# Optimization experiments

Measured on AMD Instinct MI355X. Metric: run time of the kernel, lower is better.

## Reference

```python
import jax, jax.numpy as jnp
import numpy as np

B, N, D = 8192, 50, 64


def setup_inputs() -> dict:
    key = jax.random.key(0)
    k1, k2, k3 = jax.random.split(key, 3)
    F = jax.random.normal(k1, (B, N, D), dtype=jnp.float32)
    # xavier_normal for square DxD linear: std = sqrt(2/(D+D)) = 1/sqrt(D)
    std = 1.0 / np.sqrt(D)
    K_w = jax.random.normal(k2, (D, D), dtype=jnp.float32) * std
    Q_w = jax.random.normal(k3, (D, D), dtype=jnp.float32) * std
    return {"F": F, "K_w": K_w, "Q_w": Q_w}


def reference(F, K_w, Q_w):
    # K(F): Linear with weight K_w (torch convention: x @ W^T)
    KF = jnp.einsum('bnd,ed->bne', F, K_w)          # [B,N,D]
    # S = F @ K(F)^T
    S = jnp.einsum('bnd,bmd->bnm', F, KF)           # [B,N,N]
    # out[b,n,d] = sum_m S[b,n,m] * F[b,n,d] * F[b,m,d]
    #            = F[b,n,d] * (S @ F)[b,n,d]   (algebraic fusion of the
    #              bnd,bmd->bnmd outer product + weighted sum over m)
    out = F * jnp.einsum('bnm,bmd->bnd', S, F)      # [B,N,D]
    # residual branch: Q(F)
    out = out + jnp.einsum('bnd,ed->bne', F, Q_w)
    return out
```

## Files before the change

kernel.cpp:

```cpp
#include <hip/hip_runtime.h>

typedef __attribute__((ext_vector_type(8))) short s16x8;
typedef __attribute__((ext_vector_type(4))) short s16x4;
typedef __attribute__((ext_vector_type(4))) float f32x4;

#define ST 72
#define NB 8
#define MFMA __builtin_amdgcn_mfma_f32_16x16x32_bf16

__device__ __forceinline__ short f2bf(float f) {
    unsigned u = __builtin_bit_cast(unsigned, f);
    u += 0x7FFFu + ((u >> 16) & 1u);
    return (short)(u >> 16);
}
__device__ __forceinline__ s16x8 cvt8(f32x4 a, f32x4 b) {
    s16x8 r = { f2bf(a.x), f2bf(a.y), f2bf(a.z), f2bf(a.w),
                f2bf(b.x), f2bf(b.y), f2bf(b.z), f2bf(b.w) };
    return r;
}

__global__ __launch_bounds__(256, 4) void sam3e_v2(
    const float* __restrict__ F, const float* __restrict__ Kw,
    const float* __restrict__ Qw, float* __restrict__ out)
{
    __shared__ __align__(16) short sKw[64 * ST];
    __shared__ __align__(16) short sQw[64 * ST];
    __shared__ __align__(16) short sAT[64 * ST];
    __shared__ __align__(16) short sKS[64 * ST];

    const int tid  = threadIdx.x;
    const int w    = tid >> 6;
    const int lane = tid & 63;
    const int col  = lane & 15;
    const int q    = lane >> 4;

    {
        const int e  = tid & 63;
        const int dg = tid >> 6;
        const f32x4* Kv = (const f32x4*)(Kw + e * 64 + dg * 16);
        const f32x4* Qv = (const f32x4*)(Qw + e * 64 + dg * 16);
        #pragma unroll
        for (int k = 0; k < 4; ++k) {
            f32x4 kv = Kv[k], qv = Qv[k];
            s16x4 hk = { f2bf(kv.x), f2bf(kv.y), f2bf(kv.z), f2bf(kv.w) };
            s16x4 hq = { f2bf(qv.x), f2bf(qv.y), f2bf(qv.z), f2bf(qv.w) };
            *(s16x4*)&sKw[e * ST + dg * 16 + k * 4] = hk;
            *(s16x4*)&sQw[e * ST + dg * 16 + k * 4] = hq;
        }
    }

    const int sn  = tid & 63;
    const int sdg = tid >> 6;
    const f32x4 z4 = {0.f, 0.f, 0.f, 0.f};

    int b = blockIdx.x * NB;
    f32x4 pf0 = z4, pf1 = z4, pf2 = z4, pf3 = z4;
    if (sn < 50) {
        const f32x4* Fr = (const f32x4*)(F + (size_t)b * 3200 + sn * 64 + sdg * 16);
        pf0 = Fr[0]; pf1 = Fr[1]; pf2 = Fr[2]; pf3 = Fr[3];
    }

    for (int it = 0; it < NB; ++it, ++b) {
        const float* Fb = F   + (size_t)b * 3200;
        float*       Ob = out + (size_t)b * 3200;

        __syncthreads();

        {
            const int d0 = sdg * 16;
            short h[16] = { f2bf(pf0.x), f2bf(pf0.y), f2bf(pf0.z), f2bf(pf0.w),
                            f2bf(pf1.x), f2bf(pf1.y), f2bf(pf1.z), f2bf(pf1.w),
                            f2bf(pf2.x), f2bf(pf2.y), f2bf(pf2.z), f2bf(pf2.w),
                            f2bf(pf3.x), f2bf(pf3.y), f2bf(pf3.z), f2bf(pf3.w) };
            #pragma unroll
            for (int i = 0; i < 16; ++i) sAT[(d0 + i) * ST + sn] = h[i];
        }

        s16x8 a0, a1;
        {
            const int row = 16 * w + col;
            f32x4 v0 = z4, v1 = z4, v2 = z4, v3 = z4;
            if (row < 50) {
                const f32x4* Fr = (const f32x4*)(Fb + row * 64);
                v0 = Fr[2 * q]; v1 = Fr[2 * q + 1];
                v2 = Fr[8 + 2 * q]; v3 = Fr[8 + 2 * q + 1];
            }
            a0 = cvt8(v0, v1); a1 = cvt8(v2, v3);
        }

        #pragma unroll
        for (int nt = 0; nt < 4; ++nt) {
            const short* yb = &sKw[(16 * nt + col) * ST + 8 * q];
            f32x4 acc = {0.f, 0.f, 0.f, 0.f};
            acc = MFMA(a0, *(const s16x8*)yb,        acc, 0, 0, 0);
            acc = MFMA(a1, *(const s16x8*)(yb + 32), acc, 0, 0, 0);
            #pragma unroll
            for (int r = 0; r < 4; ++r)
                sKS[(16 * w + 4 * q + r) * ST + 16 * nt + col] = f2bf(acc[r]);
        }
        __syncthreads();

        f32x4 S[4];
        #pragma unroll
        for (int nt = 0; nt < 4; ++nt) {
            const short* yb = &sKS[(16 * nt + col) * ST + 8 * q];
            f32x4 acc = {0.f, 0.f, 0.f, 0.f};
            acc = MFMA(a0, *(const s16x8*)yb,        acc, 0, 0, 0);
            acc = MFMA(a1, *(const s16x8*)(yb + 32), acc, 0, 0, 0);
            S[nt] = acc;
        }

        if (it + 1 < NB && sn < 50) {
            const f32x4* Fr = (const f32x4*)(Fb + 3200 + sn * 64 + sdg * 16);
            pf0 = Fr[0]; pf1 = Fr[1]; pf2 = Fr[2]; pf3 = Fr[3];
        }

        __syncthreads();
        #pragma unroll
        for (int nt = 0; nt < 4; ++nt)
            #pragma unroll
            for (int r = 0; r < 4; ++r)
                sKS[(16 * w + 4 * q + r) * ST + 16 * nt + col] = f2bf(S[nt][r]);
        __syncthreads();

        const short* sb = &sKS[(16 * w + col) * ST + 8 * q];
        s16x8 s0 = *(const s16x8*)sb;
        s16x8 s1 = *(const s16x8*)(sb + 32);
        #pragma unroll
        for (int nt = 0; nt < 4; ++nt) {
            const short* tb = &sAT[(16 * nt + col) * ST + 8 * q];
            const short* qb = &sQw[(16 * nt + col) * ST + 8 * q];
            f32x4 t  = {0.f, 0.f, 0.f, 0.f};
            f32x4 qa = {0.f, 0.f, 0.f, 0.f};
            t  = MFMA(s0, *(const s16x8*)tb,        t,  0, 0, 0);
            t  = MFMA(s1, *(const s16x8*)(tb + 32), t,  0, 0, 0);
            qa = MFMA(a0, *(const s16x8*)qb,        qa, 0, 0, 0);
            qa = MFMA(a1, *(const s16x8*)(qb + 32), qa, 0, 0, 0);
            #pragma unroll
            for (int r = 0; r < 4; ++r) {
                const int n = 16 * w + 4 * q + r;
                if (n < 50) {
                    const int idx = n * 64 + 16 * nt + col;
                    Ob[idx] = Fb[idx] * t[r] + qa[r];
                }
            }
        }
    }
}

extern "C" void kernel_launch(void* const* d_in, const int* in_sizes, int n_in,
                              void* d_out, int out_size, void* d_ws, size_t ws_size,
                              hipStream_t stream) {
    const float* F  = (const float*)d_in[0];
    const float* Kw = (const float*)d_in[1];
    const float* Qw = (const float*)d_in[2];
    float* out = (float*)d_out;
    sam3e_v2<<<8192 / NB, 256, 0, stream>>>(F, Kw, Qw, out);
}
```

Baseline: 221.5 us.

## Keep weight fragments in registers and use swapped-operand MFMA for contiguous LDS stores

```diff
diff --git a/kernel.cpp b/kernel.cpp
--- a/kernel.cpp
+++ b/kernel.cpp
@@ -18,15 +18,18 @@
                 f2bf(b.x), f2bf(b.y), f2bf(b.z), f2bf(b.w) };
     return r;
 }
+__device__ __forceinline__ s16x4 pack4(f32x4 a) {
+    s16x4 r = { f2bf(a.x), f2bf(a.y), f2bf(a.z), f2bf(a.w) };
+    return r;
+}
 
-__global__ __launch_bounds__(256, 4) void sam3e_v2(
+__global__ __launch_bounds__(256, 4) void sam3e_v3(
     const float* __restrict__ F, const float* __restrict__ Kw,
     const float* __restrict__ Qw, float* __restrict__ out)
 {
-    __shared__ __align__(16) short sKw[64 * ST];
-    __shared__ __align__(16) short sQw[64 * ST];
     __shared__ __align__(16) short sAT[64 * ST];
-    __shared__ __align__(16) short sKS[64 * ST];
+    __shared__ __align__(16) short sKF[64 * ST];
+    __shared__ __align__(16) short sS [64 * ST];
 
     const int tid  = threadIdx.x;
     const int w    = tid >> 6;
@@ -34,31 +37,28 @@
     const int col  = lane & 15;
     const int q    = lane >> 4;
 
-    {
-        const int e  = tid & 63;
-        const int dg = tid >> 6;
-        const f32x4* Kv = (const f32x4*)(Kw + e * 64 + dg * 16);
-        const f32x4* Qv = (const f32x4*)(Qw + e * 64 + dg * 16);
-        #pragma unroll
-        for (int k = 0; k < 4; ++k) {
-            f32x4 kv = Kv[k], qv = Qv[k];
-            s16x4 hk = { f2bf(kv.x), f2bf(kv.y), f2bf(kv.z), f2bf(kv.w) };
-            s16x4 hq = { f2bf(qv.x), f2bf(qv.y), f2bf(qv.z), f2bf(qv.w) };
-            *(s16x4*)&sKw[e * ST + dg * 16 + k * 4] = hk;
-            *(s16x4*)&sQw[e * ST + dg * 16 + k * 4] = hq;
-        }
+    s16x8 Kf[4][2], Qf[4][2];
+    #pragma unroll
+    for (int i = 0; i < 4; ++i) {
+        const float* kr = Kw + (16 * i + col) * 64 + 8 * q;
+        const float* qr = Qw + (16 * i + col) * 64 + 8 * q;
+        Kf[i][0] = cvt8(*(const f32x4*)kr,        *(const f32x4*)(kr + 4));
+        Kf[i][1] = cvt8(*(const f32x4*)(kr + 32), *(const f32x4*)(kr + 36));
+        Qf[i][0] = cvt8(*(const f32x4*)qr,        *(const f32x4*)(qr + 4));
+        Qf[i][1] = cvt8(*(const f32x4*)(qr + 32), *(const f32x4*)(qr + 36));
     }
 
-    const int sn  = tid & 63;
-    const int sdg = tid >> 6;
+    const int n4 = tid & 15;
+    const int dq = tid >> 4;
+    const int nb0 = 4 * n4;
     const f32x4 z4 = {0.f, 0.f, 0.f, 0.f};
 
     int b = blockIdx.x * NB;
-    f32x4 pf0 = z4, pf1 = z4, pf2 = z4, pf3 = z4;
-    if (sn < 50) {
-        const f32x4* Fr = (const f32x4*)(F + (size_t)b * 3200 + sn * 64 + sdg * 16);
-        pf0 = Fr[0]; pf1 = Fr[1]; pf2 = Fr[2]; pf3 = Fr[3];
-    }
+    f32x4 pf[4];
+    #pragma unroll
+    for (int rr = 0; rr < 4; ++rr)
+        pf[rr] = (nb0 + rr < 50)
+            ? *(const f32x4*)(F + (size_t)b * 3200 + (nb0 + rr) * 64 + 4 * dq) : z4;
 
     for (int it = 0; it < NB; ++it, ++b) {
         const float* Fb = F   + (size_t)b * 3200;
@@ -66,14 +66,10 @@
 
         __syncthreads();
 
-        {
-            const int d0 = sdg * 16;
-            short h[16] = { f2bf(pf0.x), f2bf(pf0.y), f2bf(pf0.z), f2bf(pf0.w),
-                            f2bf(pf1.x), f2bf(pf1.y), f2bf(pf1.z), f2bf(pf1.w),
-                            f2bf(pf2.x), f2bf(pf2.y), f2bf(pf2.z), f2bf(pf2.w),
-                            f2bf(pf3.x), f2bf(pf3.y), f2bf(pf3.z), f2bf(pf3.w) };
-            #pragma unroll
-            for (int i = 0; i < 16; ++i) sAT[(d0 + i) * ST + sn] = h[i];
+        #pragma unroll
+        for (int c = 0; c < 3 + 1; ++c) {
+            f32x4 t = { pf[0][c], pf[1][c], pf[2][c], pf[3][c] };
+            *(s16x4*)&sAT[(4 * dq + c) * ST + nb0] = pack4(t);
         }
 
         s16x8 a0, a1;
@@ -81,61 +77,51 @@
             const int row = 16 * w + col;
             f32x4 v0 = z4, v1 = z4, v2 = z4, v3 = z4;
             if (row < 50) {
-                const f32x4* Fr = (const f32x4*)(Fb + row * 64);
-                v0 = Fr[2 * q]; v1 = Fr[2 * q + 1];
-                v2 = Fr[8 + 2 * q]; v3 = Fr[8 + 2 * q + 1];
+                const float* Fr = Fb + row * 64 + 8 * q;
+                v0 = *(const f32x4*)Fr;        v1 = *(const f32x4*)(Fr + 4);
+                v2 = *(const f32x4*)(Fr + 32); v3 = *(const f32x4*)(Fr + 36);
             }
             a0 = cvt8(v0, v1); a1 = cvt8(v2, v3);
         }
 
         #pragma unroll
-        for (int nt = 0; nt < 4; ++nt) {
-            const short* yb = &sKw[(16 * nt + col) * ST + 8 * q];
-            f32x4 acc = {0.f, 0.f, 0.f, 0.f};
-            acc = MFMA(a0, *(const s16x8*)yb,        acc, 0, 0, 0);
-            acc = MFMA(a1, *(const s16x8*)(yb + 32), acc, 0, 0, 0);
-            #pragma unroll
-            for (int r = 0; r < 4; ++r)
-                sKS[(16 * w + 4 * q + r) * ST + 16 * nt + col] = f2bf(acc[r]);
+        for (int i = 0; i < 4; ++i) {
+            f32x4 acc = z4;
+            acc = MFMA(Kf[i][0], a0, acc, 0, 0, 0);
+            acc = MFMA(Kf[i][1], a1, acc, 0, 0, 0);
+            *(s16x4*)&sKF[(16 * w + col) * ST + 16 * i + 4 * q] = pack4(acc);
         }
         __syncthreads();
 
-        f32x4 S[4];
+        if (it + 1 < NB) {
+            #pragma unroll
+            for (int rr = 0; rr < 4; ++rr)
+                pf[rr] = (nb0 + rr < 50)
+                    ? *(const f32x4*)(Fb + 3200 + (nb0 + rr) * 64 + 4 * dq) : z4;
+        }
+
+        #pragma unroll
+        for (int i = 0; i < 4; ++i) {
+            s16x8 kf0 = *(const s16x8*)&sKF[(16 * i + col) * ST + 8 * q];
+            s16x8 kf1 = *(const s16x8*)&sKF[(16 * i + col) * ST + 32 + 8 * q];
+            f32x4 acc = z4;
+            acc = MFMA(kf0, a0, acc, 0, 0, 0);
+            acc = MFMA(kf1, a1, acc, 0, 0, 0);
+            *(s16x4*)&sS[(16 * w + col) * ST + 16 * i + 4 * q] = pack4(acc);
+        }
+        __syncthreads();
+
+        s16x8 s0 = *(const s16x8*)&sS[(16 * w + col) * ST + 8 * q];
+        s16x8 s1 = *(const s16x8*)&sS[(16 * w + col) * ST + 32 + 8 * q];
         #pragma unroll
         for (int nt = 0; nt < 4; ++nt) {
-            const short* yb = &sKS[(16 * nt + col) * ST + 8 * q];
-            f32x4 acc = {0.f, 0.f, 0.f, 0.f};
-            acc = MFMA(a0, *(const s16x8*)yb,        acc, 0, 0, 0);
-            acc = MFMA(a1, *(const s16x8*)(yb + 32), acc, 0, 0, 0);
-            S[nt] = acc;
-        }
-
-        if (it + 1 < NB && sn < 50) {
-            const f32x4* Fr = (const f32x4*)(Fb + 3200 + sn * 64 + sdg * 16);
-            pf0 = Fr[0]; pf1 = Fr[1]; pf2 = Fr[2]; pf3 = Fr[3];
-        }
-
-        __syncthreads();
-        #pragma unroll
-        for (int nt = 0; nt < 4; ++nt)
-            #pragma unroll
-            for (int r = 0; r < 4; ++r)
-                sKS[(16 * w + 4 * q + r) * ST + 16 * nt + col] = f2bf(S[nt][r]);
-        __syncthreads();
-
-        const short* sb = &sKS[(16 * w + col) * ST + 8 * q];
-        s16x8 s0 = *(const s16x8*)sb;
-        s16x8 s1 = *(const s16x8*)(sb + 32);
-        #pragma unroll
-        for (int nt = 0; nt < 4; ++nt) {
-            const short* tb = &sAT[(16 * nt + col) * ST + 8 * q];
-            const short* qb = &sQw[(16 * nt + col) * ST + 8 * q];
-            f32x4 t  = {0.f, 0.f, 0.f, 0.f};
-            f32x4 qa = {0.f, 0.f, 0.f, 0.f};
-            t  = MFMA(s0, *(const s16x8*)tb,        t,  0, 0, 0);
-            t  = MFMA(s1, *(const s16x8*)(tb + 32), t,  0, 0, 0);
-            qa = MFMA(a0, *(const s16x8*)qb,        qa, 0, 0, 0);
-            qa = MFMA(a1, *(const s16x8*)(qb + 32), qa, 0, 0, 0);
+            s16x8 at0 = *(const s16x8*)&sAT[(16 * nt + col) * ST + 8 * q];
+            s16x8 at1 = *(const s16x8*)&sAT[(16 * nt + col) * ST + 32 + 8 * q];
+            f32x4 t  = z4, qa = z4;
+            t  = MFMA(s0, at0, t, 0, 0, 0);
+            t  = MFMA(s1, at1, t, 0, 0, 0);
+            qa = MFMA(a0, Qf[nt][0], qa, 0, 0, 0);
+            qa = MFMA(a1, Qf[nt][1], qa, 0, 0, 0);
             #pragma unroll
             for (int r = 0; r < 4; ++r) {
                 const int n = 16 * w + 4 * q + r;
@@ -155,5 +141,5 @@
     const float* Kw = (const float*)d_in[1];
     const float* Qw = (const float*)d_in[2];
     float* out = (float*)d_out;
-    sam3e_v2<<<8192 / NB, 256, 0, stream>>>(F, Kw, Qw, out);
+    sam3e_v3<<<8192 / NB, 256, 0, stream>>>(F, Kw, Qw, out);
 }
```

New measurement: 358.0 us. 1.62x slower.
